# Performance work log

Measured on AMD Instinct MI355X. Metric: run time of the kernel, lower is better.

Reference implementation:

```python
import jax, jax.numpy as jnp
import numpy as np

N_NODES = 100000
N_EDGES = 3200000
IN_DIM = 256
OUT_DIM = 128


def setup_inputs() -> dict:
    key = jax.random.key(0)
    k1, k2, k3, k4, k5 = jax.random.split(key, 5)
    # node features
    x = jax.random.normal(k1, (N_NODES, IN_DIM), dtype=jnp.float32)
    # glorot-uniform weight as in glorot_init
    init_range = np.sqrt(6.0 / (IN_DIM + OUT_DIM)).astype(np.float32)
    weight = jax.random.uniform(k2, (IN_DIM, OUT_DIM), dtype=jnp.float32,
                                minval=-init_range, maxval=init_range)
    # sparse adjacency in COO form: adj[dst, src] = edge_weight
    edge_src = jax.random.randint(k3, (N_EDGES,), 0, N_NODES, dtype=jnp.int64)
    edge_dst = jax.random.randint(k4, (N_EDGES,), 0, N_NODES, dtype=jnp.int64)
    edge_weight = jax.random.uniform(k5, (N_EDGES,), dtype=jnp.float32)
    return {"x": x, "weight": weight, "edge_weight": edge_weight,
            "edge_src": edge_src, "edge_dst": edge_dst}


def reference(x, weight, edge_weight, edge_src, edge_dst):
    # dense feature transform: [N, in] @ [in, out] -> [N, out]
    xw = x @ weight
    # sparse adjacency matmul (adj @ xw) as gather + weighted scatter-add
    msgs = xw[edge_src] * edge_weight[:, None]           # [E, out]
    agg = jax.ops.segment_sum(msgs, edge_dst, num_segments=N_NODES)
    # fused activation
    return jax.nn.relu(agg)
```

## Files before the change

kernel.cpp:

```cpp
#include <hip/hip_runtime.h>

#define IN_DIM 256
#define OUT_DIM 128
#define BM 64
#define BKG 64

#define BSHIFT 7
#define BNODES 128
#define MAXB2 832
#define CHUNK1 3584
#define CAPB 4736
#define HCAP 2560

typedef __attribute__((ext_vector_type(4))) float floatx4;
typedef __attribute__((ext_vector_type(8))) short shortx8;

static __device__ __forceinline__ unsigned short f2bf(float f) {
  unsigned u = __float_as_uint(f);
  u += 0x7FFFu + ((u >> 16) & 1u);
  return (unsigned short)(u >> 16);
}

__global__ __launch_bounds__(256) void prep_kernel(
    const float* __restrict__ w, unsigned short* __restrict__ wt,
    int* __restrict__ btail, int nb2) {
  const int idx = blockIdx.x * 256 + threadIdx.x;
  const int k = idx >> 7;
  const int n = idx & 127;
  wt[n * IN_DIM + k] = f2bf(w[idx]);
  if (blockIdx.x == 0)
    for (int b = threadIdx.x; b < nb2; b += 256) btail[b] = 0;
}

__global__ __launch_bounds__(256) void fused_pg_kernel(
    const float* __restrict__ x, const unsigned short* __restrict__ wt,
    unsigned short* __restrict__ xw, int n_nodes,
    const int* __restrict__ esrc, const int* __restrict__ edst,
    const float* __restrict__ ew, int* __restrict__ btail,
    uint2* __restrict__ csr2, int n_edges, int nb2, int pblocks) {
  __shared__ __align__(16) union {
    struct {
      unsigned short As[BM][BKG + 8];
      unsigned short Bs[OUT_DIM][BKG + 8];
    } g;
    struct {
      uint2 srec[CHUNK1];
      int hcnt[MAXB2];
      int aux[MAXB2];
      int sh[256];
    } p;
  } sm;

  const int bid = blockIdx.x;
  const int P = pblocks;
  const int G = (int)gridDim.x - pblocks;
  bool is_part;
  int vb;
  if (P <= G) {
    if (bid < 2 * P) { is_part = !(bid & 1); vb = bid >> 1; }
    else             { is_part = false;      vb = bid - P; }
  } else {
    if (bid < 2 * G) { is_part = (bid & 1);  vb = bid >> 1; }
    else             { is_part = true;       vb = bid - G; }
  }

  const int t = threadIdx.x;

  if (is_part) {
    const int base = vb * CHUNK1;
    const int cn = min(CHUNK1, n_edges - base);

    for (int b = t; b < MAXB2; b += 256) sm.p.hcnt[b] = 0;
    __syncthreads();

    int dst[14];
    unsigned xpk[14];
#pragma unroll
    for (int i = 0; i < 14; ++i) {
      const int idx = t + i * 256;
      if (idx < cn) {
        const int e = base + idx;
        dst[i] = edst[e];
        unsigned wb = __float_as_uint(ew[e]);
        wb += 0x7FFFu + ((wb >> 16) & 1u);
        xpk[i] = ((wb >> 16) << 17) | (unsigned)esrc[e];
        atomicAdd(&sm.p.hcnt[((unsigned)dst[i]) >> BSHIFT], 1);
      } else {
        dst[i] = -1;
      }
    }
    __syncthreads();
    {
      const int b4 = 4 * t;
      int a0 = 0, a1 = 0, a2 = 0, a3 = 0;
      if (b4 < MAXB2) {
        a0 = sm.p.hcnt[b4];     a1 = sm.p.hcnt[b4 + 1];
        a2 = sm.p.hcnt[b4 + 2]; a3 = sm.p.hcnt[b4 + 3];
      }
      const int s = a0 + a1 + a2 + a3;
      sm.p.sh[t] = s;
      __syncthreads();
      for (int off = 1; off < 256; off <<= 1) {
        const int add = (t >= off) ? sm.p.sh[t - off] : 0;
        __syncthreads();
        sm.p.sh[t] += add;
        __syncthreads();
      }
      if (b4 < MAXB2) {
        int run = sm.p.sh[t] - s;
        sm.p.aux[b4] = run; run += a0;
        sm.p.aux[b4 + 1] = run; run += a1;
        sm.p.aux[b4 + 2] = run; run += a2;
        sm.p.aux[b4 + 3] = run;
      }
    }
    __syncthreads();
    for (int b = t; b < nb2; b += 256) {
      const int c = sm.p.hcnt[b];
      const int lo = sm.p.aux[b];
      int g = 0;
      if (c) g = b * CAPB + atomicAdd(&btail[b], c);
      sm.p.hcnt[b] = lo;
      sm.p.aux[b] = g - lo;
    }
    __syncthreads();
#pragma unroll
    for (int i = 0; i < 14; ++i)
      if (dst[i] >= 0) {
        const int bk = ((unsigned)dst[i]) >> BSHIFT;
        const int p = atomicAdd(&sm.p.hcnt[bk], 1);
        sm.p.srec[p] = make_uint2(xpk[i], (unsigned)dst[i]);
      }
    __syncthreads();
    for (int i = t; i < cn; i += 256) {
      const uint2 r = sm.p.srec[i];
      const int bk = r.y >> BSHIFT;
      const size_t pos = (size_t)(sm.p.aux[bk] + i);
      if (pos < (size_t)(bk + 1) * CAPB) csr2[pos] = r;
    }
  } else {
    const int wv = t >> 6;
    const int lane = t & 63;
    const int quad = lane >> 4;
    const int l16 = lane & 15;
    const int row0 = vb * BM;
    if (row0 >= n_nodes) return;

    floatx4 acc[4][2];
#pragma unroll
    for (int a = 0; a < 4; ++a)
#pragma unroll
      for (int b = 0; b < 2; ++b) acc[a][b] = (floatx4){0.f, 0.f, 0.f, 0.f};

    for (int k0 = 0; k0 < IN_DIM; k0 += BKG) {
      __syncthreads();
#pragma unroll
      for (int i = 0; i < 4; ++i) {
        const int idx = i * 256 + t;
        const int r = idx >> 4;
        const int kq = (idx & 15) * 4;
        int row = row0 + r;
        if (row >= n_nodes) row = n_nodes - 1;
        const float4 v = *(const float4*)(x + (size_t)row * IN_DIM + k0 + kq);
        ushort4 sv;
        sv.x = f2bf(v.x); sv.y = f2bf(v.y); sv.z = f2bf(v.z); sv.w = f2bf(v.w);
        *(ushort4*)&sm.g.As[r][kq] = sv;
      }
#pragma unroll
      for (int i = 0; i < 4; ++i) {
        const int idx16 = i * 256 + t;
        const int n = idx16 >> 3;
        const int off = (idx16 & 7) * 8;
        *(int4*)&sm.g.Bs[n][off] =
            *(const int4*)(wt + (size_t)n * IN_DIM + k0 + off);
      }
      __syncthreads();

#pragma unroll
      for (int kk = 0; kk < BKG; kk += 32) {
        shortx8 af[4];
#pragma unroll
        for (int tm = 0; tm < 4; ++tm)
          af[tm] = *(const shortx8*)&sm.g.As[tm * 16 + l16][kk + quad * 8];
        shortx8 bfr[2];
#pragma unroll
        for (int tn = 0; tn < 2; ++tn)
          bfr[tn] =
              *(const shortx8*)&sm.g.Bs[wv * 32 + tn * 16 + l16][kk + quad * 8];
#pragma unroll
        for (int tm = 0; tm < 4; ++tm)
#pragma unroll
          for (int tn = 0; tn < 2; ++tn)
            acc[tm][tn] = __builtin_amdgcn_mfma_f32_16x16x32_bf16(
                af[tm], bfr[tn], acc[tm][tn], 0, 0, 0);
      }
    }

#pragma unroll
    for (int tm = 0; tm < 4; ++tm)
#pragma unroll
      for (int tn = 0; tn < 2; ++tn)
#pragma unroll
        for (int r = 0; r < 4; ++r) {
          const int grow = row0 + tm * 16 + quad * 4 + r;
          const int gcol = wv * 32 + tn * 16 + l16;
          if (grow < n_nodes)
            xw[(size_t)grow * OUT_DIM + gcol] = f2bf(acc[tm][tn][r]);
        }
  }
}

struct AggSmem {
  unsigned xs[HCAP];
  int cnt[64];
  int cur[64];
  int sst[64];
  int sen[64];
  int sh[64];
};

__global__ __launch_bounds__(256, 8) void sort_agg_kernel(
    const uint2* __restrict__ csr2, const int* __restrict__ btail,
    const unsigned short* __restrict__ xw, float* __restrict__ out,
    int n_nodes) {
  __shared__ __align__(16) AggSmem sm;
  const int t = threadIdx.x;
  const int bucket = blockIdx.x >> 1;
  const int half = blockIdx.x & 1;
  const int node0 = (bucket << BSHIFT) + half * 64;
  const size_t S = (size_t)bucket * CAPB;
  const int cnt = min(btail[bucket], CAPB);

  if (t < 64) sm.cnt[t] = 0;
  __syncthreads();
  for (int i = t; i < cnt; i += 256) {
    const unsigned y = csr2[S + i].y & (BNODES - 1);
    if ((int)(y >> 6) == half) atomicAdd(&sm.cnt[y & 63], 1);
  }
  __syncthreads();
  {
    const int s = (t < 64) ? sm.cnt[t] : 0;
    if (t < 64) sm.sh[t] = s;
    __syncthreads();
    for (int off = 1; off < 64; off <<= 1) {
      const int add = (t >= off && t < 64) ? sm.sh[t - off] : 0;
      __syncthreads();
      if (t < 64) sm.sh[t] += add;
      __syncthreads();
    }
    if (t < 64) {
      const int run = sm.sh[t] - s;
      sm.cur[t] = run;
      sm.sst[t] = run;
      sm.sen[t] = run + s;
    }
  }
  __syncthreads();
  for (int i = t; i < cnt; i += 256) {
    const uint2 r = csr2[S + i];
    const unsigned y = r.y & (BNODES - 1);
    if ((int)(y >> 6) == half) {
      const int p = atomicAdd(&sm.cur[y & 63], 1);
      if (p < HCAP) sm.xs[p] = r.x;
    }
  }
  __syncthreads();

  const int g = t >> 4;
  const int lane = t & 15;
  const int d8 = lane * 8;
  const unsigned short* __restrict__ xwd = xw + d8;

  for (int nl = g; nl < 64; nl += 16) {
    const int node = node0 + nl;
    if (node >= n_nodes) continue;
    const int j0 = sm.sst[nl];
    const int j1 = min(sm.sen[nl], HCAP);

    float a0 = 0.f, a1 = 0.f, a2 = 0.f, a3 = 0.f;
    float a4 = 0.f, a5 = 0.f, a6 = 0.f, a7 = 0.f;

    int j = j0;
    for (; j + 8 <= j1; j += 8) {
      uint4 v[8];
      float wq[8];
#pragma unroll
      for (int u = 0; u < 8; ++u) {
        const unsigned p = sm.xs[j + u];
        v[u] = *(const uint4*)(xwd + (size_t)(p & 0x1FFFFu) * OUT_DIM);
        wq[u] = __uint_as_float((p >> 17) << 16);
      }
#pragma unroll
      for (int u = 0; u < 8; ++u) {
        a0 = fmaf(__uint_as_float(v[u].x << 16), wq[u], a0);
        a1 = fmaf(__uint_as_float(v[u].x & 0xFFFF0000u), wq[u], a1);
        a2 = fmaf(__uint_as_float(v[u].y << 16), wq[u], a2);
        a3 = fmaf(__uint_as_float(v[u].y & 0xFFFF0000u), wq[u], a3);
        a4 = fmaf(__uint_as_float(v[u].z << 16), wq[u], a4);
        a5 = fmaf(__uint_as_float(v[u].z & 0xFFFF0000u), wq[u], a5);
        a6 = fmaf(__uint_as_float(v[u].w << 16), wq[u], a6);
        a7 = fmaf(__uint_as_float(v[u].w & 0xFFFF0000u), wq[u], a7);
      }
    }
    for (; j < j1; ++j) {
      const unsigned p0 = sm.xs[j];
      const float w0 = __uint_as_float((p0 >> 17) << 16);
      const uint4 v0 = *(const uint4*)(xwd + (size_t)(p0 & 0x1FFFFu) * OUT_DIM);
      a0 = fmaf(__uint_as_float(v0.x << 16), w0, a0);
      a1 = fmaf(__uint_as_float(v0.x & 0xFFFF0000u), w0, a1);
      a2 = fmaf(__uint_as_float(v0.y << 16), w0, a2);
      a3 = fmaf(__uint_as_float(v0.y & 0xFFFF0000u), w0, a3);
      a4 = fmaf(__uint_as_float(v0.z << 16), w0, a4);
      a5 = fmaf(__uint_as_float(v0.z & 0xFFFF0000u), w0, a5);
      a6 = fmaf(__uint_as_float(v0.w << 16), w0, a6);
      a7 = fmaf(__uint_as_float(v0.w & 0xFFFF0000u), w0, a7);
    }

    float4 o0, o1;
    o0.x = fmaxf(a0, 0.f); o0.y = fmaxf(a1, 0.f);
    o0.z = fmaxf(a2, 0.f); o0.w = fmaxf(a3, 0.f);
    o1.x = fmaxf(a4, 0.f); o1.y = fmaxf(a5, 0.f);
    o1.z = fmaxf(a6, 0.f); o1.w = fmaxf(a7, 0.f);
    float* orow = out + (size_t)node * OUT_DIM + d8;
    *(float4*)orow = o0;
    *(float4*)(orow + 4) = o1;
  }
}

extern "C" void kernel_launch(void* const* d_in, const int* in_sizes, int n_in,
                              void* d_out, int out_size, void* d_ws,
                              size_t ws_size, hipStream_t stream) {
  const float* x    = (const float*)d_in[0];
  const float* w    = (const float*)d_in[1];
  const float* ew   = (const float*)d_in[2];
  const int*   esrc = (const int*)d_in[3];
  const int*   edst = (const int*)d_in[4];
  float* out = (float*)d_out;

  const int n_edges = in_sizes[2];
  const int n_nodes = out_size / OUT_DIM;
  const int nb2 = (n_nodes + BNODES - 1) >> BSHIFT;

  char* p = (char*)d_ws;
  unsigned short* xw = (unsigned short*)p;
  p += (size_t)n_nodes * OUT_DIM * sizeof(unsigned short);
  p = (char*)(((uintptr_t)p + 15) & ~(uintptr_t)15);
  unsigned short* wt = (unsigned short*)p;
  p += (size_t)OUT_DIM * IN_DIM * sizeof(unsigned short);
  p = (char*)(((uintptr_t)p + 15) & ~(uintptr_t)15);
  uint2* csr2 = (uint2*)p;  p += (size_t)nb2 * CAPB * sizeof(uint2);
  int* btail = (int*)p;     p += (size_t)nb2 * sizeof(int);

  prep_kernel<<<(IN_DIM * OUT_DIM) / 256, 256, 0, stream>>>(w, wt, btail, nb2);

  const int pblocks = (n_edges + CHUNK1 - 1) / CHUNK1;
  const int gblocks = (n_nodes + BM - 1) / BM;
  fused_pg_kernel<<<pblocks + gblocks, 256, 0, stream>>>(
      x, wt, xw, n_nodes, esrc, edst, ew, btail, csr2, n_edges, nb2, pblocks);

  sort_agg_kernel<<<2 * nb2, 256, 0, stream>>>(csr2, btail, xw, out, n_nodes);
}
```

Baseline: 355.8 us.

## Cache bucket records in registers, remap blocks per XCD, sort nodes by degree

The aggregation kernel now loads each bucket's records into registers once instead of reading them from global memory twice. It remaps block indices so neighbouring buckets land on the same XCD for L2 locality. It also bitonic-sorts the 64 nodes by edge count so each 16-lane group works through nodes in a more balanced order. The partition phase is retuned to 10 edges per thread, and the occupancy hint in launch bounds is dropped. The trade-off is 19 record registers per thread, which may lower occupancy, plus extra barriers for the sort.

```diff
diff --git a/kernel.cpp b/kernel.cpp
--- a/kernel.cpp
+++ b/kernel.cpp
@@ -8,9 +8,11 @@
 #define BSHIFT 7
 #define BNODES 128
 #define MAXB2 832
-#define CHUNK1 3584
+#define EPT1 10
+#define CHUNK1 2560
 #define CAPB 4736
 #define HCAP 2560
+#define RPT 19
 
 typedef __attribute__((ext_vector_type(4))) float floatx4;
 typedef __attribute__((ext_vector_type(8))) short shortx8;
@@ -73,10 +75,10 @@
     for (int b = t; b < MAXB2; b += 256) sm.p.hcnt[b] = 0;
     __syncthreads();
 
-    int dst[14];
-    unsigned xpk[14];
-#pragma unroll
-    for (int i = 0; i < 14; ++i) {
+    int dst[EPT1];
+    unsigned xpk[EPT1];
+#pragma unroll
+    for (int i = 0; i < EPT1; ++i) {
       const int idx = t + i * 256;
       if (idx < cn) {
         const int e = base + idx;
@@ -125,7 +127,7 @@
     }
     __syncthreads();
 #pragma unroll
-    for (int i = 0; i < 14; ++i)
+    for (int i = 0; i < EPT1; ++i)
       if (dst[i] >= 0) {
         const int bk = ((unsigned)dst[i]) >> BSHIFT;
         const int p = atomicAdd(&sm.p.hcnt[bk], 1);
@@ -219,23 +221,40 @@
   int sh[64];
 };
 
-__global__ __launch_bounds__(256, 8) void sort_agg_kernel(
+__global__ __launch_bounds__(256) void sort_agg_kernel(
     const uint2* __restrict__ csr2, const int* __restrict__ btail,
     const unsigned short* __restrict__ xw, float* __restrict__ out,
     int n_nodes) {
   __shared__ __align__(16) AggSmem sm;
   const int t = threadIdx.x;
-  const int bucket = blockIdx.x >> 1;
-  const int half = blockIdx.x & 1;
+
+  const int nwg = (int)gridDim.x;
+  const int q = nwg >> 3, r = nwg & 7;
+  const int xcd = blockIdx.x & 7, bix = blockIdx.x >> 3;
+  const int lb = (xcd < r ? xcd * (q + 1) : r * (q + 1) + (xcd - r) * q) + bix;
+
+  const int bucket = lb >> 1;
+  const int half = lb & 1;
   const int node0 = (bucket << BSHIFT) + half * 64;
   const size_t S = (size_t)bucket * CAPB;
   const int cnt = min(btail[bucket], CAPB);
 
+  uint2 rec[RPT];
+#pragma unroll
+  for (int k = 0; k < RPT; ++k) {
+    const int i = t + k * 256;
+    rec[k] = (i < cnt) ? csr2[S + i] : make_uint2(0u, 0xFFFFFFFFu);
+  }
+
   if (t < 64) sm.cnt[t] = 0;
   __syncthreads();
-  for (int i = t; i < cnt; i += 256) {
-    const unsigned y = csr2[S + i].y & (BNODES - 1);
-    if ((int)(y >> 6) == half) atomicAdd(&sm.cnt[y & 63], 1);
+#pragma unroll
+  for (int k = 0; k < RPT; ++k) {
+    const unsigned y = rec[k].y;
+    if (y != 0xFFFFFFFFu) {
+      const unsigned yl = y & (BNODES - 1);
+      if ((int)(yl >> 6) == half) atomicAdd(&sm.cnt[yl & 63], 1);
+    }
   }
   __syncthreads();
   {
@@ -256,22 +275,41 @@
     }
   }
   __syncthreads();
-  for (int i = t; i < cnt; i += 256) {
-    const uint2 r = csr2[S + i];
-    const unsigned y = r.y & (BNODES - 1);
-    if ((int)(y >> 6) == half) {
-      const int p = atomicAdd(&sm.cur[y & 63], 1);
-      if (p < HCAP) sm.xs[p] = r.x;
-    }
-  }
+#pragma unroll
+  for (int k = 0; k < RPT; ++k) {
+    const uint2 rr = rec[k];
+    if (rr.y != 0xFFFFFFFFu) {
+      const unsigned yl = rr.y & (BNODES - 1);
+      if ((int)(yl >> 6) == half) {
+        const int p = atomicAdd(&sm.cur[yl & 63], 1);
+        if (p < HCAP) sm.xs[p] = rr.x;
+      }
+    }
+  }
+  if (t < 64) sm.sh[t] = ((sm.sen[t] - sm.sst[t]) << 6) | t;
   __syncthreads();
+  for (int kk = 2; kk <= 64; kk <<= 1) {
+    for (int jj = kk >> 1; jj > 0; jj >>= 1) {
+      if (t < 64) {
+        const int ixj = t ^ jj;
+        if (ixj > t) {
+          const int a = sm.sh[t], b = sm.sh[ixj];
+          const bool up = ((t & kk) == 0);
+          if ((a > b) == up) { sm.sh[t] = b; sm.sh[ixj] = a; }
+        }
+      }
+      __syncthreads();
+    }
+  }
 
   const int g = t >> 4;
   const int lane = t & 15;
   const int d8 = lane * 8;
   const unsigned short* __restrict__ xwd = xw + d8;
 
-  for (int nl = g; nl < 64; nl += 16) {
+#pragma unroll
+  for (int ii = 0; ii < 4; ++ii) {
+    const int nl = sm.sh[g + (ii << 4)] & 63;
     const int node = node0 + nl;
     if (node >= n_nodes) continue;
     const int j0 = sm.sst[nl];
```

Result: no change. 350.7 us (-1.5%).
